# Performance work log

Measured on AMD Instinct MI355X. Metric: run time of the kernel, lower is better.

The kernel has to match this reference:

```python
import jax, jax.numpy as jnp
import numpy as np

BN_EPS = 1e-5


def setup_inputs() -> dict:
    key = jax.random.key(0)
    ks = jax.random.split(key, 4)
    N, C, T, V, S = 64, 64, 300, 25, 3
    x = jax.random.normal(ks[0], (N, C, T, V), dtype=jnp.float32)
    PA = jax.random.uniform(ks[1], (S, V, V), dtype=jnp.float32)
    # 1x1 conv weights per subset, branch-init scale sqrt(2/(out*1*1*branches))
    Wc = jax.random.normal(ks[2], (S, C, C), dtype=jnp.float32) * np.sqrt(2.0 / (C * S))
    bc = jnp.zeros((S, C), dtype=jnp.float32)
    gamma = jnp.ones((C,), dtype=jnp.float32)
    beta = jnp.zeros((C,), dtype=jnp.float32)
    return {"x": x, "PA": PA, "Wc": Wc, "bc": bc, "gamma": gamma, "beta": beta}


def reference(x, PA, Wc, bc, gamma, beta):
    # x: [N,C,T,V]; PA: [S,V,V]; Wc: [S,Cout,Cin]; bc: [S,Cout]
    # L2_norm: per-column L2 norm along dim=1 of each subset adjacency
    A = PA / (jnp.linalg.norm(PA, axis=1, keepdims=True) + 1e-4)  # [S,V,V]
    # For each subset: (x.view(N,CT,V) @ A[s]) then 1x1 conv, summed over subsets.
    # out[n,o,t,w] = sum_s sum_c sum_v x[n,c,t,v] * A[s,v,w] * Wc[s,o,c] + sum_s bc[s,o]
    y = jnp.einsum('nctv,svw,soc->notw', x, A, Wc)
    y = y + bc.sum(axis=0)[None, :, None, None]
    # BatchNorm2d (training-mode batch statistics) over (N,T,V) per channel
    mean = y.mean(axis=(0, 2, 3), keepdims=True)
    var = y.var(axis=(0, 2, 3), keepdims=True)
    y = (y - mean) * jax.lax.rsqrt(var + BN_EPS)
    y = y * gamma[None, :, None, None] + beta[None, :, None, None]
    # residual (identity since in_channels == out_channels) + ReLU
    return jax.nn.relu(y + x)
```

## Files before the change

### kernel.cpp

```cpp
#include <hip/hip_runtime.h>
#include <hip/hip_bf16.h>
#include <math.h>

typedef __attribute__((ext_vector_type(8))) short short8v;
typedef __attribute__((ext_vector_type(4))) float f32x4;

#define NB 64
#define CC 64
#define TT 300
#define VV 25
#define SS 3

#define AFA_BYTES 16384
#define WCF_BYTES 32768
#define YOFF_BYTES 65536

static __device__ __forceinline__ unsigned short f2bf(float f){
    union { __hip_bfloat16 h; unsigned short s; } u;
    u.h = __float2bfloat16(f);
    return u.s;
}
static __device__ __forceinline__ float bf2f(unsigned short b){
    return __uint_as_float(((unsigned)b) << 16);
}
static __device__ __forceinline__ void pack2(const f32x4& z, unsigned& d0, unsigned& d1){
    d0 = (unsigned)f2bf(z[0]) | ((unsigned)f2bf(z[1]) << 16);
    d1 = (unsigned)f2bf(z[2]) | ((unsigned)f2bf(z[3]) << 16);
}
static __device__ __forceinline__ short8v mk8(unsigned q0,unsigned q1,unsigned q2,unsigned q3){
    union { unsigned u[4]; short8v v; } x;
    x.u[0]=q0; x.u[1]=q1; x.u[2]=q2; x.u[3]=q3;
    return x.v;
}

__global__ void gcn_prep(const float* __restrict__ PA, const float* __restrict__ Wc,
                         float* __restrict__ ws)
{
    __shared__ float inv[SS][VV];
    const int tid = threadIdx.x;
    for (int i = tid; i < 1152; i += 384) if (i < 512 || i >= 1024) ws[i] = 0.f;
    if (tid < SS*VV){
        int s = tid/VV, w = tid%VV;
        float sum = 0.f;
        for (int v=0; v<VV; ++v){ float p = PA[s*VV*VV + v*VV + w]; sum = fmaf(p,p,sum); }
        inv[s][w] = 1.f/(sqrtf(sum)+1e-4f);
    }
    __syncthreads();
    {
        int s = tid/128, rem = tid%128, nt = rem/64, lane = rem%64;
        int w = nt*16 + (lane&15), g = lane>>4;
        short8v vals;
        #pragma unroll
        for (int j=0;j<8;++j){
            int v = 8*g + j;
            float f = (v<VV && w<VV) ? PA[s*VV*VV + v*VV + w]*inv[s][w] : 0.f;
            vals[j] = (short)f2bf(f);
        }
        *(short8v*)((char*)ws + AFA_BYTES + (size_t)((s*2+nt)*64 + lane)*16) = vals;
    }
    for (int fid = tid; fid < SS*4*2*64; fid += 384){
        int lane = fid & 63;
        int kt = (fid >> 6) & 1;
        int ot = (fid >> 7) & 3;
        int s  = fid >> 9;
        int o  = 16*ot + (lane & 15);
        int c0 = kt*32 + 8*(lane >> 4);
        short8v vals;
        #pragma unroll
        for (int j=0;j<8;++j) vals[j] = (short)f2bf(Wc[((size_t)s*CC + o)*CC + c0 + j]);
        *(short8v*)((char*)ws + WCF_BYTES + (size_t)fid*16) = vals;
    }
}

template<bool YB>
__global__ __launch_bounds__(256,4) void gcn_main_kernel(
    const float* __restrict__ x, const float* __restrict__ ws,
    float* __restrict__ yf32, __hip_bfloat16* __restrict__ ybf)
{
    const int lane = threadIdx.x & 63;
    const int wv   = threadIdx.x >> 6;
    const int l15  = lane & 15, g = lane >> 4;
    const int gid  = blockIdx.x * 4 + wv;
    const int n    = gid / TT;
    const int t    = gid % TT;

    short8v axf[4];
    #pragma unroll
    for (int mt=0; mt<4; ++mt){
        const int c = 16*mt + l15;
        const float* p = x + ((size_t)(n*CC + c)*TT + t)*VV + 8*g;
        short8v f;
        if (g < 3){
            float4 a = *(const float4*)p;
            float4 b = *(const float4*)(p+4);
            f[0]=(short)f2bf(a.x); f[1]=(short)f2bf(a.y); f[2]=(short)f2bf(a.z); f[3]=(short)f2bf(a.w);
            f[4]=(short)f2bf(b.x); f[5]=(short)f2bf(b.y); f[6]=(short)f2bf(b.z); f[7]=(short)f2bf(b.w);
        } else {
            f[0]=(short)f2bf(p[0]);
            f[1]=0; f[2]=0; f[3]=0; f[4]=0; f[5]=0; f[6]=0; f[7]=0;
        }
        axf[mt] = f;
    }

    const short8v* afrag = (const short8v*)((const char*)ws + AFA_BYTES);
    const short8v* wfrag = (const short8v*)((const char*)ws + WCF_BYTES);

    const f32x4 zf = {0.f,0.f,0.f,0.f};
    f32x4 yacc[4][2];
    #pragma unroll
    for (int ot=0; ot<4; ++ot){ yacc[ot][0]=zf; yacc[ot][1]=zf; }

    const int sLo = 32*(g&1) + l15;
    const int sHi = sLo + 16;
    const bool hi = (lane >= 32);

    #pragma unroll 1
    for (int s=0; s<SS; ++s){
        short8v aA0 = afrag[(s*2+0)*64 + lane];
        short8v aA1 = afrag[(s*2+1)*64 + lane];
        #pragma unroll
        for (int kt=0; kt<2; ++kt){
            f32x4 z00 = __builtin_amdgcn_mfma_f32_16x16x32_bf16(axf[2*kt+0], aA0, zf, 0,0,0);
            f32x4 z01 = __builtin_amdgcn_mfma_f32_16x16x32_bf16(axf[2*kt+0], aA1, zf, 0,0,0);
            f32x4 z10 = __builtin_amdgcn_mfma_f32_16x16x32_bf16(axf[2*kt+1], aA0, zf, 0,0,0);
            f32x4 z11 = __builtin_amdgcn_mfma_f32_16x16x32_bf16(axf[2*kt+1], aA1, zf, 0,0,0);
            unsigned pLo0n0, pLo1n0, pLo0n1, pLo1n1;
            unsigned pHi0n0, pHi1n0, pHi0n1, pHi1n1;
            pack2(z00, pLo0n0, pLo1n0);
            pack2(z01, pLo0n1, pLo1n1);
            pack2(z10, pHi0n0, pHi1n0);
            pack2(z11, pHi0n1, pHi1n1);
            unsigned a0,b0,a1,b1,a2,b2,a3,b3;
            a0=__shfl(pLo0n0,sLo); b0=__shfl(pHi0n0,sLo);
            a1=__shfl(pLo1n0,sLo); b1=__shfl(pHi1n0,sLo);
            a2=__shfl(pLo0n0,sHi); b2=__shfl(pHi0n0,sHi);
            a3=__shfl(pLo1n0,sHi); b3=__shfl(pHi1n0,sHi);
            short8v bz0 = mk8(hi?b0:a0, hi?b1:a1, hi?b2:a2, hi?b3:a3);
            a0=__shfl(pLo0n1,sLo); b0=__shfl(pHi0n1,sLo);
            a1=__shfl(pLo1n1,sLo); b1=__shfl(pHi1n1,sLo);
            a2=__shfl(pLo0n1,sHi); b2=__shfl(pHi0n1,sHi);
            a3=__shfl(pLo1n1,sHi); b3=__shfl(pHi1n1,sHi);
            short8v bz1 = mk8(hi?b0:a0, hi?b1:a1, hi?b2:a2, hi?b3:a3);
            #pragma unroll
            for (int ot=0; ot<4; ++ot){
                short8v wc = wfrag[((s*4+ot)*2+kt)*64 + lane];
                yacc[ot][0] = __builtin_amdgcn_mfma_f32_16x16x32_bf16(wc, bz0, yacc[ot][0], 0,0,0);
                yacc[ot][1] = __builtin_amdgcn_mfma_f32_16x16x32_bf16(wc, bz1, yacc[ot][1], 0,0,0);
            }
        }
    }

    #pragma unroll
    for (int ot=0; ot<4; ++ot){
        #pragma unroll
        for (int r=0; r<4; ++r){
            const int o = 16*ot + 4*g + r;
            const size_t base = (size_t)(n*CC + o)*(TT*VV) + (size_t)t*VV;
            if (YB){
                ybf[base + l15] = __float2bfloat16(yacc[ot][0][r]);
                if (l15 < VV-16) ybf[base + 16 + l15] = __float2bfloat16(yacc[ot][1][r]);
            } else {
                yf32[base + l15] = yacc[ot][0][r];
                if (l15 < VV-16) yf32[base + 16 + l15] = yacc[ot][1][r];
            }
        }
    }
}

template<bool YB>
__global__ __launch_bounds__(256) void gcn_stat_kernel(
    const float* __restrict__ yf, const unsigned short* __restrict__ ybf,
    float* __restrict__ ws)
{
    __shared__ float red[2][4];
    const int b = blockIdx.x;
    float s1 = 0.f, s2 = 0.f;
    if (YB){
        const uint2* p = (const uint2*)(ybf + (size_t)b*(TT*VV));
        for (int i = threadIdx.x; i < TT*VV/4; i += 256){
            uint2 u = p[i];
            float a0=bf2f((unsigned short)(u.x&0xffff)), a1=bf2f((unsigned short)(u.x>>16));
            float a2=bf2f((unsigned short)(u.y&0xffff)), a3=bf2f((unsigned short)(u.y>>16));
            s1 += (a0+a1)+(a2+a3);
            s2 = fmaf(a0,a0,fmaf(a1,a1,fmaf(a2,a2,fmaf(a3,a3,s2))));
        }
    } else {
        const float4* p = (const float4*)(yf + (size_t)b*(TT*VV));
        for (int i = threadIdx.x; i < TT*VV/4; i += 256){
            float4 v = p[i];
            s1 += (v.x+v.y)+(v.z+v.w);
            s2 = fmaf(v.x,v.x,fmaf(v.y,v.y,fmaf(v.z,v.z,fmaf(v.w,v.w,s2))));
        }
    }
    #pragma unroll
    for (int m=1; m<64; m<<=1){ s1 += __shfl_xor(s1,m); s2 += __shfl_xor(s2,m); }
    const int wv = threadIdx.x >> 6;
    if ((threadIdx.x & 63) == 0){ red[0][wv]=s1; red[1][wv]=s2; }
    __syncthreads();
    if (threadIdx.x == 0){
        float S1 = red[0][0]+red[0][1]+red[0][2]+red[0][3];
        float S2 = red[1][0]+red[1][1]+red[1][2]+red[1][3];
        int o = b & (CC-1);
        atomicAdd(&ws[o*8],     S1);
        atomicAdd(&ws[o*8 + 4], S2);
    }
}

__global__ void gcn_finalize_kernel(const float* __restrict__ gamma,
                                    const float* __restrict__ beta,
                                    float* __restrict__ ws)
{
    const int o = threadIdx.x;
    if (o < CC) {
        const float cnt = (float)(NB * TT * VV);
        const float mean = ws[o*8] / cnt;
        const float var  = ws[o*8 + 4] / cnt - mean * mean;
        const float sc   = gamma[o] * rsqrtf(var + 1e-5f);
        ws[1024 + o] = sc;
        ws[1088 + o] = beta[o] - mean * sc;
    }
}

template<bool YB>
__global__ __launch_bounds__(256) void gcn_bn_relu_kernel(
    const float* __restrict__ x, float* __restrict__ out,
    const float* __restrict__ ws, const unsigned short* __restrict__ ybf)
{
    const int total4 = NB * CC * TT * VV / 4;
    const int per_c4 = TT * VV / 4;
    for (int i = blockIdx.x * 256 + threadIdx.x; i < total4; i += gridDim.x * 256) {
        const int c = (i / per_c4) & (CC - 1);
        const float sc = ws[1024 + c];
        const float sh = ws[1088 + c];
        float4 yv;
        if (YB){
            uint2 yb = *(const uint2*)&ybf[4*i];
            yv.x = bf2f((unsigned short)(yb.x & 0xffff));
            yv.y = bf2f((unsigned short)(yb.x >> 16));
            yv.z = bf2f((unsigned short)(yb.y & 0xffff));
            yv.w = bf2f((unsigned short)(yb.y >> 16));
        } else {
            yv = reinterpret_cast<float4*>(out)[i];
        }
        float4 xv = reinterpret_cast<const float4*>(x)[i];
        float4 r;
        r.x = fmaxf(fmaf(yv.x, sc, sh) + xv.x, 0.f);
        r.y = fmaxf(fmaf(yv.y, sc, sh) + xv.y, 0.f);
        r.z = fmaxf(fmaf(yv.z, sc, sh) + xv.z, 0.f);
        r.w = fmaxf(fmaf(yv.w, sc, sh) + xv.w, 0.f);
        reinterpret_cast<float4*>(out)[i] = r;
    }
}

extern "C" void kernel_launch(void* const* d_in, const int* in_sizes, int n_in,
                              void* d_out, int out_size, void* d_ws, size_t ws_size,
                              hipStream_t stream)
{
    const float* x     = (const float*)d_in[0];
    const float* PA    = (const float*)d_in[1];
    const float* Wc    = (const float*)d_in[2];
    const float* gamma = (const float*)d_in[4];
    const float* beta  = (const float*)d_in[5];
    float* out = (float*)d_out;
    float* ws  = (float*)d_ws;

    const size_t ybytes = (size_t)NB*CC*TT*VV*2;
    const bool yb = ws_size >= (size_t)YOFF_BYTES + ybytes;
    __hip_bfloat16* ybf = (__hip_bfloat16*)((char*)d_ws + YOFF_BYTES);

    gcn_prep<<<1, 384, 0, stream>>>(PA, Wc, ws);
    if (yb){
        gcn_main_kernel<true><<<NB*TT/4, 256, 0, stream>>>(x, ws, out, ybf);
        gcn_stat_kernel<true><<<NB*CC, 256, 0, stream>>>(out, (const unsigned short*)ybf, ws);
        gcn_finalize_kernel<<<1, 64, 0, stream>>>(gamma, beta, ws);
        gcn_bn_relu_kernel<true><<<2048, 256, 0, stream>>>(x, out, ws, (const unsigned short*)ybf);
    } else {
        gcn_main_kernel<false><<<NB*TT/4, 256, 0, stream>>>(x, ws, out, ybf);
        gcn_stat_kernel<false><<<NB*CC, 256, 0, stream>>>(out, (const unsigned short*)ybf, ws);
        gcn_finalize_kernel<<<1, 64, 0, stream>>>(gamma, beta, ws);
        gcn_bn_relu_kernel<false><<<2048, 256, 0, stream>>>(x, out, ws, (const unsigned short*)ybf);
    }
}
```

Baseline: 131.7 us.

## Fuse BN statistics into GEMM kernel and stage x tile through LDS

Removes the separate statistics kernel. Each main-kernel block now reduces per-channel sum and sum-of-squares from the bf16 outputs held in LDS and atomically adds them into per-sample slots, which the finalize kernel then sums. The x input is loaded cooperatively with coalesced float4 reads into a padded LDS tile covering four time steps, instead of per-lane strided global loads. This avoids re-reading the intermediate y, at the cost of extra LDS traffic, barriers and more atomics. Occupancy hint raised to 8.

```diff
diff --git a/kernel.cpp b/kernel.cpp
--- a/kernel.cpp
+++ b/kernel.cpp
@@ -10,10 +10,12 @@
 #define TT 300
 #define VV 25
 #define SS 3
-
-#define AFA_BYTES 16384
-#define WCF_BYTES 32768
-#define YOFF_BYTES 65536
+#define TB 4
+#define TBLK (TT/TB)
+
+#define AFA_BYTES 36864
+#define WCF_BYTES 49152
+#define YOFF_BYTES 131072
 
 static __device__ __forceinline__ unsigned short f2bf(float f){
     union { __hip_bfloat16 h; unsigned short s; } u;
@@ -38,7 +40,7 @@
 {
     __shared__ float inv[SS][VV];
     const int tid = threadIdx.x;
-    for (int i = tid; i < 1152; i += 384) if (i < 512 || i >= 1024) ws[i] = 0.f;
+    for (int i = tid; i < 8192; i += 384) ws[i] = 0.f;
     if (tid < SS*VV){
         int s = tid/VV, w = tid%VV;
         float sum = 0.f;
@@ -72,34 +74,48 @@
     }
 }
 
+#define XPITCH 36
+
 template<bool YB>
-__global__ __launch_bounds__(256,4) void gcn_main_kernel(
-    const float* __restrict__ x, const float* __restrict__ ws,
+__global__ __launch_bounds__(256,8) void gcn_main_kernel(
+    const float* __restrict__ x, float* __restrict__ ws,
     float* __restrict__ yf32, __hip_bfloat16* __restrict__ ybf)
 {
-    const int lane = threadIdx.x & 63;
-    const int wv   = threadIdx.x >> 6;
+    __shared__ __align__(16) unsigned short lds[256*XPITCH];
+
+    const int tid  = threadIdx.x;
+    const int lane = tid & 63;
+    const int wv   = tid >> 6;
     const int l15  = lane & 15, g = lane >> 4;
-    const int gid  = blockIdx.x * 4 + wv;
-    const int n    = gid / TT;
-    const int t    = gid % TT;
+    const int n    = blockIdx.x / TBLK;
+    const int t0   = (blockIdx.x % TBLK) * TB;
+    const int t    = t0 + wv;
+
+    #pragma unroll
+    for (int k = 25; k < 32; ++k) lds[tid*XPITCH + k] = 0;
+
+    const float4* x4 = (const float4*)(x + ((size_t)n*CC*TT + t0)*VV);
+    for (int i4 = tid; i4 < CC*TB*VV/4; i4 += 256){
+        int c = i4 / (TB*VV/4);
+        int j = i4 % (TB*VV/4);
+        float4 v4 = x4[c*(TT*VV/4) + j];
+        float vals[4] = {v4.x, v4.y, v4.z, v4.w};
+        int e = 4*j;
+        #pragma unroll
+        for (int k=0;k<4;++k){
+            int ee = e+k;
+            lds[((ee/VV)*64 + c)*XPITCH + (ee%VV)] = f2bf(vals[k]);
+        }
+    }
+    __syncthreads();
 
     short8v axf[4];
     #pragma unroll
     for (int mt=0; mt<4; ++mt){
-        const int c = 16*mt + l15;
-        const float* p = x + ((size_t)(n*CC + c)*TT + t)*VV + 8*g;
-        short8v f;
-        if (g < 3){
-            float4 a = *(const float4*)p;
-            float4 b = *(const float4*)(p+4);
-            f[0]=(short)f2bf(a.x); f[1]=(short)f2bf(a.y); f[2]=(short)f2bf(a.z); f[3]=(short)f2bf(a.w);
-            f[4]=(short)f2bf(b.x); f[5]=(short)f2bf(b.y); f[6]=(short)f2bf(b.z); f[7]=(short)f2bf(b.w);
-        } else {
-            f[0]=(short)f2bf(p[0]);
-            f[1]=0; f[2]=0; f[3]=0; f[4]=0; f[5]=0; f[6]=0; f[7]=0;
-        }
-        axf[mt] = f;
+        const unsigned short* rp = &lds[(wv*64 + 16*mt + l15)*XPITCH + 8*g];
+        uint2 lo = *(const uint2*)rp;
+        uint2 hi = *(const uint2*)(rp + 4);
+        axf[mt] = mk8(lo.x, lo.y, hi.x, hi.y);
     }
 
     const short8v* afrag = (const short8v*)((const char*)ws + AFA_BYTES);
@@ -150,59 +166,42 @@
         }
     }
 
+    __syncthreads();
     #pragma unroll
     for (int ot=0; ot<4; ++ot){
         #pragma unroll
         for (int r=0; r<4; ++r){
             const int o = 16*ot + 4*g + r;
             const size_t base = (size_t)(n*CC + o)*(TT*VV) + (size_t)t*VV;
-            if (YB){
-                ybf[base + l15] = __float2bfloat16(yacc[ot][0][r]);
-                if (l15 < VV-16) ybf[base + 16 + l15] = __float2bfloat16(yacc[ot][1][r]);
-            } else {
-                yf32[base + l15] = yacc[ot][0][r];
-                if (l15 < VV-16) yf32[base + 16 + l15] = yacc[ot][1][r];
+            unsigned short b0 = f2bf(yacc[ot][0][r]);
+            lds[o*100 + wv*25 + l15] = b0;
+            if (YB) ybf[base + l15] = __float2bfloat16(yacc[ot][0][r]);
+            else    yf32[base + l15] = yacc[ot][0][r];
+            if (l15 < VV-16){
+                unsigned short b1 = f2bf(yacc[ot][1][r]);
+                lds[o*100 + wv*25 + 16 + l15] = b1;
+                if (YB) ybf[base + 16 + l15] = __float2bfloat16(yacc[ot][1][r]);
+                else    yf32[base + 16 + l15] = yacc[ot][1][r];
             }
         }
     }
-}
-
-template<bool YB>
-__global__ __launch_bounds__(256) void gcn_stat_kernel(
-    const float* __restrict__ yf, const unsigned short* __restrict__ ybf,
-    float* __restrict__ ws)
-{
-    __shared__ float red[2][4];
-    const int b = blockIdx.x;
-    float s1 = 0.f, s2 = 0.f;
-    if (YB){
-        const uint2* p = (const uint2*)(ybf + (size_t)b*(TT*VV));
-        for (int i = threadIdx.x; i < TT*VV/4; i += 256){
-            uint2 u = p[i];
-            float a0=bf2f((unsigned short)(u.x&0xffff)), a1=bf2f((unsigned short)(u.x>>16));
-            float a2=bf2f((unsigned short)(u.y&0xffff)), a3=bf2f((unsigned short)(u.y>>16));
-            s1 += (a0+a1)+(a2+a3);
-            s2 = fmaf(a0,a0,fmaf(a1,a1,fmaf(a2,a2,fmaf(a3,a3,s2))));
-        }
-    } else {
-        const float4* p = (const float4*)(yf + (size_t)b*(TT*VV));
-        for (int i = threadIdx.x; i < TT*VV/4; i += 256){
-            float4 v = p[i];
-            s1 += (v.x+v.y)+(v.z+v.w);
-            s2 = fmaf(v.x,v.x,fmaf(v.y,v.y,fmaf(v.z,v.z,fmaf(v.w,v.w,s2))));
-        }
-    }
-    #pragma unroll
-    for (int m=1; m<64; m<<=1){ s1 += __shfl_xor(s1,m); s2 += __shfl_xor(s2,m); }
-    const int wv = threadIdx.x >> 6;
-    if ((threadIdx.x & 63) == 0){ red[0][wv]=s1; red[1][wv]=s2; }
-    __syncthreads();
-    if (threadIdx.x == 0){
-        float S1 = red[0][0]+red[0][1]+red[0][2]+red[0][3];
-        float S2 = red[1][0]+red[1][1]+red[1][2]+red[1][3];
-        int o = b & (CC-1);
-        atomicAdd(&ws[o*8],     S1);
-        atomicAdd(&ws[o*8 + 4], S2);
+    __syncthreads();
+
+    {
+        const int o = tid >> 2, q = tid & 3;
+        float s1 = 0.f, s2 = 0.f;
+        #pragma unroll
+        for (int k=0; k<VV; ++k){
+            float v = bf2f(lds[o*100 + q*25 + k]);
+            s1 += v;
+            s2 = fmaf(v, v, s2);
+        }
+        s1 += __shfl_xor(s1,1); s1 += __shfl_xor(s1,2);
+        s2 += __shfl_xor(s2,1); s2 += __shfl_xor(s2,2);
+        if (q == 0){
+            atomicAdd(&ws[n*128 + o],      s1);
+            atomicAdd(&ws[n*128 + 64 + o], s2);
+        }
     }
 }
 
@@ -212,12 +211,17 @@
 {
     const int o = threadIdx.x;
     if (o < CC) {
+        float s = 0.f, q = 0.f;
+        for (int n = 0; n < NB; ++n){
+            s += ws[n*128 + o];
+            q += ws[n*128 + 64 + o];
+        }
         const float cnt = (float)(NB * TT * VV);
-        const float mean = ws[o*8] / cnt;
-        const float var  = ws[o*8 + 4] / cnt - mean * mean;
+        const float mean = s / cnt;
+        const float var  = q / cnt - mean * mean;
         const float sc   = gamma[o] * rsqrtf(var + 1e-5f);
-        ws[1024 + o] = sc;
-        ws[1088 + o] = beta[o] - mean * sc;
+        ws[8192 + o] = sc;
+        ws[8256 + o] = beta[o] - mean * sc;
     }
 }
 
@@ -230,8 +234,8 @@
     const int per_c4 = TT * VV / 4;
     for (int i = blockIdx.x * 256 + threadIdx.x; i < total4; i += gridDim.x * 256) {
         const int c = (i / per_c4) & (CC - 1);
-        const float sc = ws[1024 + c];
-        const float sh = ws[1088 + c];
+        const float sc = ws[8192 + c];
+        const float sh = ws[8256 + c];
         float4 yv;
         if (YB){
             uint2 yb = *(const uint2*)&ybf[4*i];
@@ -270,13 +274,11 @@
 
     gcn_prep<<<1, 384, 0, stream>>>(PA, Wc, ws);
     if (yb){
-        gcn_main_kernel<true><<<NB*TT/4, 256, 0, stream>>>(x, ws, out, ybf);
-        gcn_stat_kernel<true><<<NB*CC, 256, 0, stream>>>(out, (const unsigned short*)ybf, ws);
+        gcn_main_kernel<true><<<NB*TBLK, 256, 0, stream>>>(x, ws, out, ybf);
         gcn_finalize_kernel<<<1, 64, 0, stream>>>(gamma, beta, ws);
         gcn_bn_relu_kernel<true><<<2048, 256, 0, stream>>>(x, out, ws, (const unsigned short*)ybf);
     } else {
-        gcn_main_kernel<false><<<NB*TT/4, 256, 0, stream>>>(x, ws, out, ybf);
-        gcn_stat_kernel<false><<<NB*CC, 256, 0, stream>>>(out, (const unsigned short*)ybf, ws);
+        gcn_main_kernel<false><<<NB*TBLK, 256, 0, stream>>>(x, ws, out, ybf);
         gcn_finalize_kernel<<<1, 64, 0, stream>>>(gamma, beta, ws);
         gcn_bn_relu_kernel<false><<<2048, 256, 0, stream>>>(x, out, ws, (const unsigned short*)ybf);
     }
```

Measured after the change: 178.9 us. 1.36x slower.
